# Performance work log

Hardware: AMD Instinct MI355X
Metric: run time of the kernel (lower is better)

Reference implementation:

```python
import jax, jax.numpy as jnp
import numpy as np

BS, EMB, RES = 256, 768, 14
N_MASKS, HID, OUT, N_PROJ = 16, 4096, 256, 4
BN_EPS = 1e-5


def setup_inputs() -> dict:
    key = jax.random.key(0)
    ks = jax.random.split(key, 8)
    x = jax.random.normal(ks[0], (BS, EMB, RES, RES), jnp.float32)
    # binary ROI masks over the 14x14 = 196 patch grid
    masks = (jax.random.uniform(ks[1], (BS, N_MASKS, RES * RES)) < 0.3).astype(jnp.float32)
    projection_idx = jax.random.randint(ks[2], (N_MASKS,), 0, N_PROJ, jnp.int32)
    mask_ids = jax.random.randint(ks[3], (BS, N_MASKS), 0, 100, jnp.int32)
    # stacked params for the N_PROJ MLP projectors
    W1 = jax.random.normal(ks[4], (N_PROJ, EMB, HID), jnp.float32) * 0.02
    b1 = jnp.zeros((N_PROJ, HID), jnp.float32)
    gamma = jnp.ones((N_PROJ, HID), jnp.float32)
    beta = jnp.zeros((N_PROJ, HID), jnp.float32)
    W2 = jax.random.normal(ks[5], (N_PROJ, HID, OUT), jnp.float32) * 0.02
    b2 = jnp.zeros((N_PROJ, OUT), jnp.float32)
    return {"x": x, "masks": masks, "projection_idx": projection_idx,
            "mask_ids": mask_ids, "W1": W1, "b1": b1, "gamma": gamma,
            "beta": beta, "W2": W2, "b2": b2}


def reference(x, masks, projection_idx, mask_ids, W1, b1, gamma, beta, W2, b2):
    bs, emb, hx, hy = x.shape
    # [bs, emb, hx, hy] -> [bs, hw, emb]
    emb_local = jnp.transpose(x, (0, 2, 3, 1)).reshape(bs, hx * hy, emb)
    # mask-normalized pooling:  pooled[b,n,:] = mean of embeddings inside mask n
    area = masks.sum(axis=-1, keepdims=True)
    smpl = masks / jnp.maximum(area, 1.0)
    pooled = smpl @ emb_local                       # [bs, n_masks, emb]
    # dense dispatch: run EVERY projector over all pooled tokens (as original)
    h = jnp.einsum('bne,peh->pbnh', pooled, W1) + b1[:, None, None, :]
    # BatchNorm1d in training mode over flattened (bs*n_masks) batch, per projector
    mu = h.mean(axis=(1, 2), keepdims=True)
    var = jnp.mean(jnp.square(h - mu), axis=(1, 2), keepdims=True)  # biased var
    h = (h - mu) * jax.lax.rsqrt(var + BN_EPS) * gamma[:, None, None, :] + beta[:, None, None, :]
    h = jax.nn.relu(h)
    o = jnp.einsum('pbnh,pho->pbno', h, W2) + b2[:, None, None, :]   # [P, bs, n, out]
    # keep only projector projection_idx[n] for mask-slot n (disjoint selection)
    n_proj = W1.shape[0]
    sel = (projection_idx[None, :] == jnp.arange(n_proj)[:, None]).astype(o.dtype)  # [P, n]
    xs = (o * sel[:, None, :, None]).sum(axis=0)     # [bs, n_masks, out]
    return (xs, mask_ids)
```

## Files before the change

kernel.cpp:

```cpp
#include <hip/hip_runtime.h>
#include <hip/hip_bf16.h>

#define BS 256
#define EMB 768
#define HW 196
#define NMASK 16
#define HID 4096
#define OUT 256
#define NPROJ 4
#define MROWS 4096

typedef __attribute__((ext_vector_type(8))) short bf16x8;
typedef __attribute__((ext_vector_type(4))) float f32x4;
typedef __attribute__((ext_vector_type(8))) unsigned short u16x8;

__device__ inline float bf2f(unsigned short u) {
    unsigned int x = ((unsigned int)u) << 16;
    return __builtin_bit_cast(float, x);
}
__device__ inline short f2bfs(float f) {
    return __builtin_bit_cast(short, __float2bfloat16(f));
}

#define GL16(gptr, lptr)                                                     \
    __builtin_amdgcn_global_load_lds(                                        \
        (const __attribute__((address_space(1))) void*)(gptr),               \
        (__attribute__((address_space(3))) void*)(lptr), 16, 0, 0)

__global__ __launch_bounds__(256) void pool_mfma(
    const float* __restrict__ x, const float* __restrict__ masks,
    __hip_bfloat16* __restrict__ pooledG)
{
    __shared__ __align__(16) short afr[7 * 64 * 8];
    __shared__ float inv[NMASK];
    const int ec = blockIdx.x, b = blockIdx.y, tid = threadIdx.x;
    const float* mb = masks + (size_t)b * NMASK * HW;

    for (int s = tid; s < 7 * 64; s += 256) {
        int m = s & 15, kb = ((s >> 4) & 3) * 8 + (s >> 6) * 32;
        short v[8];
        #pragma unroll
        for (int j = 0; j < 8; ++j) {
            int kk = kb + j;
            v[j] = (kk < HW) ? f2bfs(mb[m * HW + kk]) : (short)0;
        }
        #pragma unroll
        for (int j = 0; j < 8; ++j) afr[s * 8 + j] = v[j];
    }
    if (tid >= 192) {
        int l = tid - 192, m = l >> 2, q = l & 3;
        float a = 0.f;
        for (int hw = q; hw < HW; hw += 4) a += mb[m * HW + hw];
        a += __shfl_xor(a, 1);
        a += __shfl_xor(a, 2);
        if (q == 0) inv[m] = 1.0f / fmaxf(a, 1.0f);
    }
    __syncthreads();

    const int lane = tid & 63, w = tid >> 6;
    const int lc = lane & 15, l4 = lane >> 4;
    const int ebase = ec * 192 + w * 48;
    const bf16x8* afv = (const bf16x8*)afr;
    f32x4 acc[3] = {};

    const float* xb0 = x + ((size_t)b * EMB + ebase + lc) * HW;

    for (int kc = 0; kc < 6; ++kc) {
        bf16x8 af = afv[kc * 64 + lane];
        float4 u[3][2];
        #pragma unroll
        for (int t = 0; t < 3; ++t) {
            const float* xr = xb0 + (size_t)(t * 16) * HW + kc * 32 + l4 * 8;
            u[t][0] = *(const float4*)(xr);
            u[t][1] = *(const float4*)(xr + 4);
        }
        #pragma unroll
        for (int t = 0; t < 3; ++t) {
            bf16x8 bf;
            bf[0] = f2bfs(u[t][0].x); bf[1] = f2bfs(u[t][0].y);
            bf[2] = f2bfs(u[t][0].z); bf[3] = f2bfs(u[t][0].w);
            bf[4] = f2bfs(u[t][1].x); bf[5] = f2bfs(u[t][1].y);
            bf[6] = f2bfs(u[t][1].z); bf[7] = f2bfs(u[t][1].w);
            acc[t] = __builtin_amdgcn_mfma_f32_16x16x32_bf16(af, bf, acc[t], 0, 0, 0);
        }
    }
    {
        bf16x8 af = afv[6 * 64 + lane];
        #pragma unroll
        for (int t = 0; t < 3; ++t) {
            bf16x8 bf = {};
            if (l4 == 0) {
                float4 u0 = *(const float4*)(xb0 + (size_t)(t * 16) * HW + 192);
                bf[0] = f2bfs(u0.x); bf[1] = f2bfs(u0.y);
                bf[2] = f2bfs(u0.z); bf[3] = f2bfs(u0.w);
            }
            acc[t] = __builtin_amdgcn_mfma_f32_16x16x32_bf16(af, bf, acc[t], 0, 0, 0);
        }
    }

    #pragma unroll
    for (int t = 0; t < 3; ++t) {
        int e = ebase + t * 16 + lc;
        #pragma unroll
        for (int j = 0; j < 4; ++j) {
            int m = l4 * 4 + j;
            pooledG[((size_t)m * 256 + b) * EMB + e] =
                __float2bfloat16(acc[t][j] * inv[m]);
        }
    }
}

__global__ __launch_bounds__(256) void transpose_cvt(
    const float* __restrict__ src, __hip_bfloat16* __restrict__ dst, int R, int C)
{
    __shared__ float tile[64][65];
    const float* s = src + (size_t)blockIdx.z * R * C;
    __hip_bfloat16* d = dst + (size_t)blockIdx.z * R * C;
    const int c0 = blockIdx.x * 64, r0 = blockIdx.y * 64, tid = threadIdx.x;
    for (int i = tid; i < 4096; i += 256) {
        int r = i >> 6, c = i & 63;
        tile[r][c] = s[(size_t)(r0 + r) * C + c0 + c];
    }
    __syncthreads();
    for (int i = tid; i < 4096; i += 256) {
        int c = i >> 6, r = i & 63;
        d[(size_t)(c0 + c) * R + r0 + r] = __float2bfloat16(tile[r][c]);
    }
}

__global__ __launch_bounds__(256) void transpose_pg(
    const __hip_bfloat16* __restrict__ src, __hip_bfloat16* __restrict__ dst)
{
    __shared__ __hip_bfloat16 tile[64][65];
    const int c0 = blockIdx.x * 64, r0 = blockIdx.y * 64, tid = threadIdx.x;
    for (int i = tid; i < 4096; i += 256) {
        int r = i >> 6, c = i & 63;
        tile[r][c] = src[(size_t)(r0 + r) * EMB + c0 + c];
    }
    __syncthreads();
    for (int i = tid; i < 4096; i += 256) {
        int c = i >> 6, r = i & 63;
        dst[(size_t)(c0 + c) * MROWS + r0 + r] = tile[r][c];
    }
}

__global__ __launch_bounds__(256) void meanpool(
    const __hip_bfloat16* __restrict__ PT, float* __restrict__ mp)
{
    const int e = blockIdx.x, tid = threadIdx.x;
    const u16x8* p = (const u16x8*)(PT + (size_t)e * MROWS);
    u16x8 v1 = p[tid], v2 = p[tid + 256];
    float s = 0.f;
    #pragma unroll
    for (int j = 0; j < 8; ++j) s += bf2f((unsigned short)v1[j]) + bf2f((unsigned short)v2[j]);
    #pragma unroll
    for (int o = 1; o < 64; o <<= 1) s += __shfl_xor(s, o);
    __shared__ float wsum[4];
    if ((tid & 63) == 0) wsum[tid >> 6] = s;
    __syncthreads();
    if (tid == 0) mp[e] = (wsum[0] + wsum[1] + wsum[2] + wsum[3]) * (1.0f / 4096.0f);
}

__global__ __launch_bounds__(256) void cgemm(
    const __hip_bfloat16* __restrict__ PT, float* __restrict__ Cpart)
{
    __shared__ __align__(16) __hip_bfloat16 As[128 * 32];
    __shared__ __align__(16) __hip_bfloat16 Bs[128 * 32];
    const int tid = threadIdx.x, lane = tid & 63, wid = tid >> 6;
    const int n0 = blockIdx.x * 128, m0 = blockIdx.y * 128, kbase = blockIdx.z * 512;
    float* Cp = Cpart + (size_t)blockIdx.z * EMB * EMB;
    const int wr = wid >> 1, wc = wid & 1;
    const int l4 = lane >> 4, lc = lane & 15;

    f32x4 acc[4][4] = {};
    for (int k0 = kbase; k0 < kbase + 512; k0 += 32) {
        __syncthreads();
        #pragma unroll
        for (int r = 0; r < 2; ++r) {
            int t = r * 256 + tid;
            int row = t >> 2, ko = (t & 3) * 8;
            GL16(PT + (size_t)(m0 + row) * MROWS + k0 + ko, &As[(r * 256 + wid * 64) * 8]);
        }
        #pragma unroll
        for (int r = 0; r < 2; ++r) {
            int t = r * 256 + tid;
            int row = t >> 2, ko = (t & 3) * 8;
            GL16(PT + (size_t)(n0 + row) * MROWS + k0 + ko, &Bs[(r * 256 + wid * 64) * 8]);
        }
        __syncthreads();
        const bf16x8* Av = (const bf16x8*)As;
        const bf16x8* Bv = (const bf16x8*)Bs;
        bf16x8 a[4], b[4];
        #pragma unroll
        for (int m = 0; m < 4; ++m) a[m] = Av[(wr * 64 + m * 16 + lc) * 4 + l4];
        #pragma unroll
        for (int n = 0; n < 4; ++n) b[n] = Bv[(wc * 64 + n * 16 + lc) * 4 + l4];
        #pragma unroll
        for (int m = 0; m < 4; ++m)
            #pragma unroll
            for (int n = 0; n < 4; ++n)
                acc[m][n] = __builtin_amdgcn_mfma_f32_16x16x32_bf16(a[m], b[n], acc[m][n], 0, 0, 0);
    }
    #pragma unroll
    for (int m = 0; m < 4; ++m)
        #pragma unroll
        for (int n = 0; n < 4; ++n)
            #pragma unroll
            for (int j = 0; j < 4; ++j) {
                int row = m0 + wr * 64 + m * 16 + l4 * 4 + j;
                int col = n0 + wc * 64 + n * 16 + lc;
                Cp[(size_t)row * EMB + col] = acc[m][n][j];
            }
}

__global__ __launch_bounds__(256) void cvt_c(
    const float* __restrict__ Cpart, __hip_bfloat16* __restrict__ Cbf)
{
    int i = (blockIdx.x * 256 + threadIdx.x) * 4;
    float sx = 0.f, sy = 0.f, sz = 0.f, sw = 0.f;
    #pragma unroll
    for (int kz = 0; kz < 8; ++kz) {
        float4 v = *(const float4*)(Cpart + (size_t)kz * EMB * EMB + i);
        sx += v.x; sy += v.y; sz += v.z; sw += v.w;
    }
    const float s = 1.0f / 4096.0f;
    Cbf[i + 0] = __float2bfloat16(sx * s);
    Cbf[i + 1] = __float2bfloat16(sy * s);
    Cbf[i + 2] = __float2bfloat16(sz * s);
    Cbf[i + 3] = __float2bfloat16(sw * s);
}

__global__ __launch_bounds__(256) void ugemm(
    const __hip_bfloat16* __restrict__ W1T, const __hip_bfloat16* __restrict__ Cbf,
    const float* __restrict__ mp,
    float* __restrict__ Eh2p, float* __restrict__ Mup)
{
    __shared__ __align__(16) __hip_bfloat16 As[128 * 32];
    __shared__ __align__(16) __hip_bfloat16 Bs[128 * 32];
    const int tid = threadIdx.x, lane = tid & 63, wid = tid >> 6;
    const int n0 = blockIdx.x * 128, m0 = blockIdx.y * 128, p = blockIdx.z;
    const __hip_bfloat16* Ap = W1T + (size_t)p * HID * EMB;
    const int wr = wid >> 1, wc = wid & 1;
    const int l4 = lane >> 4, lc = lane & 15;

    f32x4 acc[4][4] = {};
    for (int k0 = 0; k0 < EMB; k0 += 32) {
        __syncthreads();
        #pragma unroll
        for (int r = 0; r < 2; ++r) {
            int t = r * 256 + tid;
            int row = t >> 2, ko = (t & 3) * 8;
            GL16(Ap + (size_t)(m0 + row) * EMB + k0 + ko, &As[(r * 256 + wid * 64) * 8]);
        }
        #pragma unroll
        for (int r = 0; r < 2; ++r) {
            int t = r * 256 + tid;
            int row = t >> 2, ko = (t & 3) * 8;
            GL16(Cbf + (size_t)(n0 + row) * EMB + k0 + ko, &Bs[(r * 256 + wid * 64) * 8]);
        }
        __syncthreads();
        const bf16x8* Av = (const bf16x8*)As;
        const bf16x8* Bv = (const bf16x8*)Bs;
        bf16x8 a[4], b[4];
        #pragma unroll
        for (int m = 0; m < 4; ++m) a[m] = Av[(wr * 64 + m * 16 + lc) * 4 + l4];
        #pragma unroll
        for (int n = 0; n < 4; ++n) b[n] = Bv[(wc * 64 + n * 16 + lc) * 4 + l4];
        #pragma unroll
        for (int m = 0; m < 4; ++m)
            #pragma unroll
            for (int n = 0; n < 4; ++n)
                acc[m][n] = __builtin_amdgcn_mfma_f32_16x16x32_bf16(a[m], b[n], acc[m][n], 0, 0, 0);
    }

    float mpv[4];
    #pragma unroll
    for (int n = 0; n < 4; ++n) mpv[n] = mp[n0 + wc * 64 + n * 16 + lc];
    #pragma unroll
    for (int m = 0; m < 4; ++m) {
        #pragma unroll
        for (int j = 0; j < 4; ++j) {
            int row = m0 + wr * 64 + m * 16 + l4 * 4 + j;
            const __hip_bfloat16* wrow = Ap + (size_t)row * EMB;
            float e2 = 0.f, mu = 0.f;
            #pragma unroll
            for (int n = 0; n < 4; ++n) {
                int col = n0 + wc * 64 + n * 16 + lc;
                float wv = bf2f(__builtin_bit_cast(unsigned short, wrow[col]));
                e2 += acc[m][n][j] * wv;
                mu += mpv[n] * wv;
            }
            e2 += __shfl_xor(e2, 1); e2 += __shfl_xor(e2, 2);
            e2 += __shfl_xor(e2, 4); e2 += __shfl_xor(e2, 8);
            mu += __shfl_xor(mu, 1); mu += __shfl_xor(mu, 2);
            mu += __shfl_xor(mu, 4); mu += __shfl_xor(mu, 8);
            if (lc == 0) {
                size_t idx = (((size_t)blockIdx.x * 2 + wc) * NPROJ + p) * HID + row;
                Eh2p[idx] = e2;
                Mup [idx] = mu;
            }
        }
    }
}

__global__ __launch_bounds__(256) void finalize(
    const float* __restrict__ Eh2p, const float* __restrict__ Mup,
    const float* __restrict__ gamma, const float* __restrict__ beta,
    float* __restrict__ sbuf, float* __restrict__ tbuf)
{
    int i = blockIdx.x * 256 + threadIdx.x;
    float e2 = 0.f, mu = 0.f;
    #pragma unroll
    for (int bx = 0; bx < 12; ++bx) {
        e2 += Eh2p[bx * (NPROJ * HID) + i];
        mu += Mup [bx * (NPROJ * HID) + i];
    }
    float var = e2 - mu * mu;
    float is  = rsqrtf(fmaxf(var, 0.0f) + 1e-5f);
    float sc  = gamma[i] * is;
    sbuf[i] = sc;
    tbuf[i] = beta[i] - mu * sc;
}

__global__ __launch_bounds__(256) void gemm1_sel(
    const __hip_bfloat16* __restrict__ A, const __hip_bfloat16* __restrict__ W1T,
    const int* __restrict__ proj,
    const float* __restrict__ sbuf, const float* __restrict__ tbuf,
    __hip_bfloat16* __restrict__ hrelu)
{
    __shared__ __align__(16) __hip_bfloat16 As[128 * 32];
    __shared__ __align__(16) __hip_bfloat16 Bs[128 * 32];
    const int tid = threadIdx.x, lane = tid & 63, wid = tid >> 6;
    const int n0 = blockIdx.x * 128, m0 = blockIdx.y * 128;
    const int p = proj[blockIdx.y >> 1];
    const __hip_bfloat16* Bp = W1T + (size_t)p * HID * EMB;
    const int wr = wid >> 1, wc = wid & 1;
    const int l4 = lane >> 4, lc = lane & 15;

    f32x4 acc[4][4] = {};
    for (int k0 = 0; k0 < EMB; k0 += 32) {
        __syncthreads();
        #pragma unroll
        for (int r = 0; r < 2; ++r) {
            int t = r * 256 + tid;
            int row = t >> 2, ko = (t & 3) * 8;
            GL16(A + (size_t)(m0 + row) * EMB + k0 + ko, &As[(r * 256 + wid * 64) * 8]);
        }
        #pragma unroll
        for (int r = 0; r < 2; ++r) {
            int t = r * 256 + tid;
            int row = t >> 2, ko = (t & 3) * 8;
            GL16(Bp + (size_t)(n0 + row) * EMB + k0 + ko, &Bs[(r * 256 + wid * 64) * 8]);
        }
        __syncthreads();
        const bf16x8* Av = (const bf16x8*)As;
        const bf16x8* Bv = (const bf16x8*)Bs;
        bf16x8 a[4], b[4];
        #pragma unroll
        for (int m = 0; m < 4; ++m) a[m] = Av[(wr * 64 + m * 16 + lc) * 4 + l4];
        #pragma unroll
        for (int n = 0; n < 4; ++n) b[n] = Bv[(wc * 64 + n * 16 + lc) * 4 + l4];
        #pragma unroll
        for (int m = 0; m < 4; ++m)
            #pragma unroll
            for (int n = 0; n < 4; ++n)
                acc[m][n] = __builtin_amdgcn_mfma_f32_16x16x32_bf16(a[m], b[n], acc[m][n], 0, 0, 0);
    }

    #pragma unroll
    for (int n = 0; n < 4; ++n) {
        int col = n0 + wc * 64 + n * 16 + lc;
        float s = sbuf[p * HID + col];
        float t = tbuf[p * HID + col];
        #pragma unroll
        for (int m = 0; m < 4; ++m)
            #pragma unroll
            for (int j = 0; j < 4; ++j) {
                int row = m0 + wr * 64 + m * 16 + l4 * 4 + j;
                float v = fmaxf(acc[m][n][j] * s + t, 0.0f);
                hrelu[(size_t)row * HID + col] = __float2bfloat16(v);
            }
    }
}

__global__ __launch_bounds__(256) void gemm2(
    const __hip_bfloat16* __restrict__ Hn, const __hip_bfloat16* __restrict__ W2T,
    const int* __restrict__ proj, float* __restrict__ Opart)
{
    __shared__ __align__(16) __hip_bfloat16 As[64 * 32];
    __shared__ __align__(16) __hip_bfloat16 Bs[64 * 32];
    const int tid = threadIdx.x, lane = tid & 63, wid = tid >> 6;
    const int nmask = blockIdx.x;
    const int bc    = blockIdx.y;
    const int ct    = blockIdx.z >> 2, kz = blockIdx.z & 3;
    const int p = proj[nmask];
    const __hip_bfloat16* Ap = Hn + (size_t)(nmask * 256 + bc * 64) * HID;
    const __hip_bfloat16* Bp = W2T + ((size_t)p * OUT + ct * 64) * HID;
    float* Op = Opart + (size_t)kz * MROWS * OUT;
    const int wr = wid >> 1, wc = wid & 1;
    const int l4 = lane >> 4, lc = lane & 15;

    f32x4 acc[2][2] = {};
    for (int k0 = kz * 1024; k0 < kz * 1024 + 1024; k0 += 32) {
        __syncthreads();
        {
            int row = tid >> 2, ko = (tid & 3) * 8;
            GL16(Ap + (size_t)row * HID + k0 + ko, &As[(wid * 64) * 8]);
            GL16(Bp + (size_t)row * HID + k0 + ko, &Bs[(wid * 64) * 8]);
        }
        __syncthreads();
        const bf16x8* Av = (const bf16x8*)As;
        const bf16x8* Bv = (const bf16x8*)Bs;
        bf16x8 a[2], b[2];
        a[0] = Av[(wr * 32 +      lc) * 4 + l4];
        a[1] = Av[(wr * 32 + 16 + lc) * 4 + l4];
        b[0] = Bv[(wc * 32 +      lc) * 4 + l4];
        b[1] = Bv[(wc * 32 + 16 + lc) * 4 + l4];
        #pragma unroll
        for (int m = 0; m < 2; ++m)
            #pragma unroll
            for (int n = 0; n < 2; ++n)
                acc[m][n] = __builtin_amdgcn_mfma_f32_16x16x32_bf16(a[m], b[n], acc[m][n], 0, 0, 0);
    }

    #pragma unroll
    for (int m = 0; m < 2; ++m)
        #pragma unroll
        for (int n = 0; n < 2; ++n)
            #pragma unroll
            for (int j = 0; j < 4; ++j) {
                int bb = bc * 64 + wr * 32 + m * 16 + l4 * 4 + j;
                int oc = ct * 64 + wc * 32 + n * 16 + lc;
                Op[((size_t)bb * NMASK + nmask) * OUT + oc] = acc[m][n][j];
            }
}

__global__ __launch_bounds__(256) void reduce_out(
    const float* __restrict__ Opart, const float* __restrict__ b2,
    const int* __restrict__ proj, const int* __restrict__ mids,
    float* __restrict__ out)
{
    int i = (blockIdx.x * 256 + threadIdx.x) * 4;
    float sx = 0.f, sy = 0.f, sz = 0.f, sw = 0.f;
    #pragma unroll
    for (int kz = 0; kz < 4; ++kz) {
        float4 v = *(const float4*)(Opart + (size_t)kz * MROWS * OUT + i);
        sx += v.x; sy += v.y; sz += v.z; sw += v.w;
    }
    int nm = (i >> 8) & 15;
    int p  = proj[nm];
    float4 bv = *(const float4*)(b2 + p * OUT + (i & 255));
    float4 r;
    r.x = sx + bv.x; r.y = sy + bv.y; r.z = sz + bv.z; r.w = sw + bv.w;
    *(float4*)(out + i) = r;
    if (blockIdx.x < 16) {
        int t = blockIdx.x * 256 + threadIdx.x;
        out[(size_t)MROWS * OUT + t] = (float)mids[t];
    }
}

extern "C" void kernel_launch(void* const* d_in, const int* in_sizes, int n_in,
                              void* d_out, int out_size, void* d_ws, size_t ws_size,
                              hipStream_t stream)
{
    const float* x     = (const float*)d_in[0];
    const float* masks = (const float*)d_in[1];
    const int*   proj  = (const int*)d_in[2];
    const int*   mids  = (const int*)d_in[3];
    const float* W1    = (const float*)d_in[4];
    const float* gamma = (const float*)d_in[6];
    const float* beta  = (const float*)d_in[7];
    const float* W2    = (const float*)d_in[8];
    const float* b2    = (const float*)d_in[9];
    float* out = (float*)d_out;

    char* ws = (char*)d_ws;
    __hip_bfloat16* pooledG = (__hip_bfloat16*)(ws);
    __hip_bfloat16* W1T     = (__hip_bfloat16*)(ws + 6291456);
    __hip_bfloat16* W2T     = (__hip_bfloat16*)(ws + 31457280);
    float*          mp      = (float*)(ws + 39845888);
    float*          Eh2p    = (float*)(ws + 39848960);
    float*          Mup     = (float*)(ws + 40635392);
    float*          sbuf    = (float*)(ws + 41421824);
    float*          tbuf    = (float*)(ws + 41487360);
    char* R = ws + 41552896;
    __hip_bfloat16* pooledT = (__hip_bfloat16*)(R);
    float*          Cpart   = (float*)(R + 6291456);
    __hip_bfloat16* Cbf     = (__hip_bfloat16*)(R + 25165824);
    __hip_bfloat16* hrelu   = (__hip_bfloat16*)(R);
    float*          Opart   = (float*)(R + 33554432);

    pool_mfma<<<dim3(4, BS), 256, 0, stream>>>(x, masks, pooledG);
    transpose_cvt<<<dim3(HID / 64, EMB / 64, NPROJ), 256, 0, stream>>>(W1, W1T, EMB, HID);
    transpose_cvt<<<dim3(OUT / 64, HID / 64, NPROJ), 256, 0, stream>>>(W2, W2T, HID, OUT);
    transpose_pg<<<dim3(EMB / 64, MROWS / 64), 256, 0, stream>>>(pooledG, pooledT);
    meanpool<<<EMB, 256, 0, stream>>>(pooledT, mp);
    cgemm<<<dim3(6, 6, 8), 256, 0, stream>>>(pooledT, Cpart);
    cvt_c<<<(EMB * EMB) / 1024, 256, 0, stream>>>(Cpart, Cbf);
    ugemm<<<dim3(6, 32, 4), 256, 0, stream>>>(W1T, Cbf, mp, Eh2p, Mup);
    finalize<<<(NPROJ * HID) / 256, 256, 0, stream>>>(Eh2p, Mup, gamma, beta, sbuf, tbuf);
    gemm1_sel<<<dim3(HID / 128, MROWS / 128), 256, 0, stream>>>(pooledG, W1T, proj, sbuf, tbuf, hrelu);
    gemm2<<<dim3(NMASK, BS / 64, 16), 256, 0, stream>>>(hrelu, W2T, proj, Opart);
    reduce_out<<<(MROWS * OUT) / 1024, 256, 0, stream>>>(Opart, b2, proj, mids, out);
}
```

Before: 211.6 us.

## Enlarge GEMM tiles with double-buffered swizzled LDS pipeline in gemm1 and larger gemm2 tiles

gemm1_sel moves to 256x256 output tiles with 512 threads and a 64-wide K step. Its LDS is double-buffered with XOR-swizzled chunk placement, so the next tile loads while MFMAs run, and MFMA sections get raised wave priority. gemm2 moves from 64x64 to 128x128 tiles, which halves the grid's per-tile operand reloads. The aim is more data reuse per LDS load and fewer barrier stalls. In exchange, the large LDS footprint and high register use limit occupancy, and the grids get smaller.

Measured after the change: 204.8 us. 1.03x faster.

```diff
diff --git a/kernel.cpp b/kernel.cpp
--- a/kernel.cpp
+++ b/kernel.cpp
@@ -322,62 +322,99 @@
     tbuf[i] = beta[i] - mu * sc;
 }
 
-__global__ __launch_bounds__(256) void gemm1_sel(
+__global__ __launch_bounds__(512, 2) void gemm1_sel(
     const __hip_bfloat16* __restrict__ A, const __hip_bfloat16* __restrict__ W1T,
     const int* __restrict__ proj,
     const float* __restrict__ sbuf, const float* __restrict__ tbuf,
     __hip_bfloat16* __restrict__ hrelu)
 {
-    __shared__ __align__(16) __hip_bfloat16 As[128 * 32];
-    __shared__ __align__(16) __hip_bfloat16 Bs[128 * 32];
-    const int tid = threadIdx.x, lane = tid & 63, wid = tid >> 6;
-    const int n0 = blockIdx.x * 128, m0 = blockIdx.y * 128;
-    const int p = proj[blockIdx.y >> 1];
-    const __hip_bfloat16* Bp = W1T + (size_t)p * HID * EMB;
-    const int wr = wid >> 1, wc = wid & 1;
-    const int l4 = lane >> 4, lc = lane & 15;
-
-    f32x4 acc[4][4] = {};
-    for (int k0 = 0; k0 < EMB; k0 += 32) {
-        __syncthreads();
-        #pragma unroll
-        for (int r = 0; r < 2; ++r) {
-            int t = r * 256 + tid;
-            int row = t >> 2, ko = (t & 3) * 8;
-            GL16(A + (size_t)(m0 + row) * EMB + k0 + ko, &As[(r * 256 + wid * 64) * 8]);
-        }
-        #pragma unroll
-        for (int r = 0; r < 2; ++r) {
-            int t = r * 256 + tid;
-            int row = t >> 2, ko = (t & 3) * 8;
-            GL16(Bp + (size_t)(n0 + row) * EMB + k0 + ko, &Bs[(r * 256 + wid * 64) * 8]);
-        }
-        __syncthreads();
-        const bf16x8* Av = (const bf16x8*)As;
-        const bf16x8* Bv = (const bf16x8*)Bs;
-        bf16x8 a[4], b[4];
-        #pragma unroll
-        for (int m = 0; m < 4; ++m) a[m] = Av[(wr * 64 + m * 16 + lc) * 4 + l4];
-        #pragma unroll
-        for (int n = 0; n < 4; ++n) b[n] = Bv[(wc * 64 + n * 16 + lc) * 4 + l4];
-        #pragma unroll
-        for (int m = 0; m < 4; ++m)
-            #pragma unroll
-            for (int n = 0; n < 4; ++n)
-                acc[m][n] = __builtin_amdgcn_mfma_f32_16x16x32_bf16(a[m], b[n], acc[m][n], 0, 0, 0);
-    }
-
-    #pragma unroll
-    for (int n = 0; n < 4; ++n) {
-        int col = n0 + wc * 64 + n * 16 + lc;
+    __shared__ __align__(16) short LS[2][32768];
+    const int tid = threadIdx.x, lane = tid & 63, w = tid >> 6;
+    const int wr = w >> 2, wc = w & 3;
+    const int lc = lane & 15, l4 = lane >> 4;
+    const int n0 = blockIdx.x * 256, m0 = blockIdx.y * 256;
+    const int p = proj[blockIdx.y];
+    const __hip_bfloat16* Ag = A;
+    const __hip_bfloat16* Bg = W1T + (size_t)p * HID * EMB;
+    const bf16x8* LSv = (const bf16x8*)LS;
+
+    const int st_row_l = lane >> 3;
+    const int st_cs    = lane & 7;
+    auto STAGE = [&](int sbf, int t) {
+        #pragma unroll
+        for (int ab = 0; ab < 2; ++ab) {
+            const __hip_bfloat16* g = ab ? Bg : Ag;
+            const int rbase = ab ? n0 : m0;
+            #pragma unroll
+            for (int i = 0; i < 4; ++i) {
+                int row = w * 32 + i * 8 + st_row_l;
+                int csl = st_cs ^ (row & 7);
+                const __hip_bfloat16* src =
+                    g + (size_t)(rbase + row) * EMB + t * 64 + csl * 8;
+                char* dst = (char*)LS + ab * 32768 + sbf * 65536 + w * 4096 + i * 1024;
+                GL16(src, dst);
+            }
+        }
+    };
+
+    f32x4 acc[8][4] = {};
+
+    STAGE(0, 0);
+    asm volatile("s_waitcnt vmcnt(0)" ::: "memory");
+    __builtin_amdgcn_s_barrier();
+
+    for (int t = 0; t < 12; ++t) {
+        const int buf = t & 1;
+        if (t + 1 < 12) STAGE(buf ^ 1, t + 1);
+
+        const int vbA = buf * 4096;
+        const int vbB = buf * 4096 + 2048;
+
+        bf16x8 bfr[4][2];
+        #pragma unroll
+        for (int nf = 0; nf < 4; ++nf) {
+            int row_b = wc * 64 + nf * 16 + lc;
+            #pragma unroll
+            for (int ks = 0; ks < 2; ++ks)
+                bfr[nf][ks] = LSv[vbB + row_b * 8 + ((ks * 4 + l4) ^ (row_b & 7))];
+        }
+        #pragma unroll
+        for (int q = 0; q < 4; ++q) {
+            bf16x8 afr[2][2];
+            #pragma unroll
+            for (int mf2 = 0; mf2 < 2; ++mf2) {
+                int row_a = wr * 128 + (q * 2 + mf2) * 16 + lc;
+                #pragma unroll
+                for (int ks = 0; ks < 2; ++ks)
+                    afr[mf2][ks] = LSv[vbA + row_a * 8 + ((ks * 4 + l4) ^ (row_a & 7))];
+            }
+            __builtin_amdgcn_s_setprio(1);
+            #pragma unroll
+            for (int mf2 = 0; mf2 < 2; ++mf2)
+                #pragma unroll
+                for (int nf = 0; nf < 4; ++nf)
+                    #pragma unroll
+                    for (int ks = 0; ks < 2; ++ks)
+                        acc[q * 2 + mf2][nf] = __builtin_amdgcn_mfma_f32_16x16x32_bf16(
+                            afr[mf2][ks], bfr[nf][ks], acc[q * 2 + mf2][nf], 0, 0, 0);
+            __builtin_amdgcn_s_setprio(0);
+        }
+
+        asm volatile("s_waitcnt vmcnt(0)" ::: "memory");
+        __builtin_amdgcn_s_barrier();
+    }
+
+    #pragma unroll
+    for (int nf = 0; nf < 4; ++nf) {
+        int col = n0 + wc * 64 + nf * 16 + lc;
         float s = sbuf[p * HID + col];
-        float t = tbuf[p * HID + col];
-        #pragma unroll
-        for (int m = 0; m < 4; ++m)
+        float tt = tbuf[p * HID + col];
+        #pragma unroll
+        for (int mf = 0; mf < 8; ++mf)
             #pragma unroll
             for (int j = 0; j < 4; ++j) {
-                int row = m0 + wr * 64 + m * 16 + l4 * 4 + j;
-                float v = fmaxf(acc[m][n][j] * s + t, 0.0f);
+                int row = m0 + wr * 128 + mf * 16 + l4 * 4 + j;
+                float v = fmaxf(acc[mf][nf][j] * s + tt, 0.0f);
                 hrelu[(size_t)row * HID + col] = __float2bfloat16(v);
             }
     }
@@ -387,50 +424,57 @@
     const __hip_bfloat16* __restrict__ Hn, const __hip_bfloat16* __restrict__ W2T,
     const int* __restrict__ proj, float* __restrict__ Opart)
 {
-    __shared__ __align__(16) __hip_bfloat16 As[64 * 32];
-    __shared__ __align__(16) __hip_bfloat16 Bs[64 * 32];
+    __shared__ __align__(16) __hip_bfloat16 As[128 * 32];
+    __shared__ __align__(16) __hip_bfloat16 Bs[128 * 32];
     const int tid = threadIdx.x, lane = tid & 63, wid = tid >> 6;
     const int nmask = blockIdx.x;
     const int bc    = blockIdx.y;
     const int ct    = blockIdx.z >> 2, kz = blockIdx.z & 3;
     const int p = proj[nmask];
-    const __hip_bfloat16* Ap = Hn + (size_t)(nmask * 256 + bc * 64) * HID;
-    const __hip_bfloat16* Bp = W2T + ((size_t)p * OUT + ct * 64) * HID;
+    const __hip_bfloat16* Ap = Hn + (size_t)(nmask * 256 + bc * 128) * HID;
+    const __hip_bfloat16* Bp = W2T + ((size_t)p * OUT + ct * 128) * HID;
     float* Op = Opart + (size_t)kz * MROWS * OUT;
     const int wr = wid >> 1, wc = wid & 1;
     const int l4 = lane >> 4, lc = lane & 15;
 
-    f32x4 acc[2][2] = {};
+    f32x4 acc[4][4] = {};
     for (int k0 = kz * 1024; k0 < kz * 1024 + 1024; k0 += 32) {
         __syncthreads();
-        {
-            int row = tid >> 2, ko = (tid & 3) * 8;
-            GL16(Ap + (size_t)row * HID + k0 + ko, &As[(wid * 64) * 8]);
-            GL16(Bp + (size_t)row * HID + k0 + ko, &Bs[(wid * 64) * 8]);
+        #pragma unroll
+        for (int r = 0; r < 2; ++r) {
+            int t = r * 256 + tid;
+            int row = t >> 2, ko = (t & 3) * 8;
+            GL16(Ap + (size_t)row * HID + k0 + ko, &As[(r * 256 + wid * 64) * 8]);
+        }
+        #pragma unroll
+        for (int r = 0; r < 2; ++r) {
+            int t = r * 256 + tid;
+            int row = t >> 2, ko = (t & 3) * 8;
+            GL16(Bp + (size_t)row * HID + k0 + ko, &Bs[(r * 256 + wid * 64) * 8]);
         }
         __syncthreads();
         const bf16x8* Av = (const bf16x8*)As;
         const bf16x8* Bv = (const bf16x8*)Bs;
-        bf16x8 a[2], b[2];
-        a[0] = Av[(wr * 32 +      lc) * 4 + l4];
-        a[1] = Av[(wr * 32 + 16 + lc) * 4 + l4];
-        b[0] = Bv[(wc * 32 +      lc) * 4 + l4];
-        b[1] = Bv[(wc * 32 + 16 + lc) * 4 + l4];
-        #pragma unroll
-        for (int m = 0; m < 2; ++m)
-            #pragma unroll
-            for (int n = 0; n < 2; ++n)
+        bf16x8 a[4], b[4];
+        #pragma unroll
+        for (int m = 0; m < 4; ++m) a[m] = Av[(wr * 64 + m * 16 + lc) * 4 + l4];
+        #pragma unroll
+        for (int n = 0; n < 4; ++n) b[n] = Bv[(wc * 64 + n * 16 + lc) * 4 + l4];
+        #pragma unroll
+        for (int m = 0; m < 4; ++m)
+            #pragma unroll
+            for (int n = 0; n < 4; ++n)
                 acc[m][n] = __builtin_amdgcn_mfma_f32_16x16x32_bf16(a[m], b[n], acc[m][n], 0, 0, 0);
     }
 
     #pragma unroll
-    for (int m = 0; m < 2; ++m)
-        #pragma unroll
-        for (int n = 0; n < 2; ++n)
+    for (int m = 0; m < 4; ++m)
+        #pragma unroll
+        for (int n = 0; n < 4; ++n)
             #pragma unroll
             for (int j = 0; j < 4; ++j) {
-                int bb = bc * 64 + wr * 32 + m * 16 + l4 * 4 + j;
-                int oc = ct * 64 + wc * 32 + n * 16 + lc;
+                int bb = bc * 128 + wr * 64 + m * 16 + l4 * 4 + j;
+                int oc = ct * 128 + wc * 64 + n * 16 + lc;
                 Op[((size_t)bb * NMASK + nmask) * OUT + oc] = acc[m][n][j];
             }
 }
@@ -499,7 +543,7 @@
     cvt_c<<<(EMB * EMB) / 1024, 256, 0, stream>>>(Cpart, Cbf);
     ugemm<<<dim3(6, 32, 4), 256, 0, stream>>>(W1T, Cbf, mp, Eh2p, Mup);
     finalize<<<(NPROJ * HID) / 256, 256, 0, stream>>>(Eh2p, Mup, gamma, beta, sbuf, tbuf);
-    gemm1_sel<<<dim3(HID / 128, MROWS / 128), 256, 0, stream>>>(pooledG, W1T, proj, sbuf, tbuf, hrelu);
-    gemm2<<<dim3(NMASK, BS / 64, 16), 256, 0, stream>>>(hrelu, W2T, proj, Opart);
+    gemm1_sel<<<dim3(HID / 256, MROWS / 256), 512, 0, stream>>>(pooledG, W1T, proj, sbuf, tbuf, hrelu);
+    gemm2<<<dim3(NMASK, 2, 8), 256, 0, stream>>>(hrelu, W2T, proj, Opart);
     reduce_out<<<(MROWS * OUT) / 1024, 256, 0, stream>>>(Opart, b2, proj, mids, out);
 }
```
